# Optimization experiments

Measured on AMD Instinct MI355X. Metric: run time of the kernel, lower is better.

The kernel has to match this reference:

```python
import jax, jax.numpy as jnp
import numpy as np

HIDDEN = 1024
NHEAD = 16
HEAD_DIM = HIDDEN // NHEAD
B, S = 2, 2048


def setup_inputs() -> dict:
    key = jax.random.key(0)
    ks = jax.random.split(key, 10)
    scale = 1.0 / np.sqrt(HIDDEN)
    inp = {
        "x": jax.random.normal(ks[0], (B, S, HIDDEN), dtype=jnp.float32),
        "mask": jax.random.randint(ks[1], (B, S), 0, 2).astype(bool),
        "Wq": jax.random.normal(ks[2], (HIDDEN, HIDDEN), dtype=jnp.float32) * scale,
        "bq": jnp.zeros((HIDDEN,), dtype=jnp.float32),
        "Wk": jax.random.normal(ks[3], (HIDDEN, HIDDEN), dtype=jnp.float32) * scale,
        "bk": jnp.zeros((HIDDEN,), dtype=jnp.float32),
        "Wv": jax.random.normal(ks[4], (HIDDEN, HIDDEN), dtype=jnp.float32) * scale,
        "bv": jnp.zeros((HIDDEN,), dtype=jnp.float32),
        "Wo": jax.random.normal(ks[5], (HIDDEN, HIDDEN), dtype=jnp.float32) * scale,
        "bo": jnp.zeros((HIDDEN,), dtype=jnp.float32),
    }
    return inp


def reference(x, mask, Wq, bq, Wk, bk, Wv, bv, Wo, bo):
    B_, S_, H = x.shape
    # QKV projections (torch Linear: x @ W.T + b), split into heads -> [B, nhead, S, head_dim]
    def split_heads(t):
        return t.reshape(B_, S_, NHEAD, HEAD_DIM).transpose(0, 2, 1, 3)

    q = split_heads(x @ Wq.T + bq)
    k = split_heads(x @ Wk.T + bk)
    v = split_heads(x @ Wv.T + bv)

    # scaled dot-product scores: [B, nhead, S, S]
    energy = jnp.einsum("bhqd,bhkd->bhqk", q, k) / jnp.sqrt(jnp.float32(HEAD_DIM))

    # combined padding + diagonal-exclusion mask: mask keys where mask[b,k] is True,
    # but never mask the diagonal (self) position
    eye = jnp.eye(S_, dtype=bool)  # [S, S]
    attn_mask = mask[:, None, None, :] & ~eye[None, None, :, :]  # [B, 1, S, S] broadcast over heads
    energy = jnp.where(attn_mask, -jnp.inf, energy)

    attention = jax.nn.softmax(energy, axis=-1)
    out = jnp.einsum("bhqk,bhkd->bhqd", attention, v)  # [B, nhead, S, head_dim]
    out = out.transpose(0, 2, 1, 3).reshape(B_, S_, H)
    return out @ Wo.T + bo
```

## Files before the change

### kernel.cpp

```cpp
#include <hip/hip_runtime.h>

typedef __attribute__((ext_vector_type(8))) short short8;
typedef __attribute__((ext_vector_type(4))) float f32x4;
typedef __attribute__((ext_vector_type(16))) float f32x16;
typedef __attribute__((ext_vector_type(4))) unsigned short ushort4v;

#define HIDDEN 1024
#define NHEAD 16
#define HD 64
#define BATCH 2
#define SEQ 2048
#define MROWS (BATCH * SEQ)
#define QSCALE 0.18033688011112042f

__device__ __forceinline__ unsigned short f2b(float f) {
  union { float f; unsigned u; } v; v.f = f;
  unsigned r = v.u + 0x7fffu + ((v.u >> 16) & 1u);
  return (unsigned short)(r >> 16);
}

__device__ __forceinline__ unsigned cvt_pk_bf16(float lo, float hi) {
  unsigned r;
  asm("v_cvt_pk_bf16_f32 %0, %1, %2" : "=v"(r) : "v"(lo), "v"(hi));
  return r;
}

__device__ __forceinline__ float fexp2(float x) {
#if __has_builtin(__builtin_amdgcn_exp2f)
  return __builtin_amdgcn_exp2f(x);
#else
  return exp2f(x);
#endif
}

__device__ __forceinline__ void gll16(const void* g, void* l) {
  __builtin_amdgcn_global_load_lds(
      (__attribute__((address_space(1))) void*)g,
      (__attribute__((address_space(3))) void*)l, 16, 0, 0);
}

__global__ void prep_kernel(const float* __restrict__ x,
                            const float* __restrict__ Wq,
                            const float* __restrict__ Wk,
                            const float* __restrict__ Wv,
                            const float* __restrict__ Wo,
                            unsigned short* __restrict__ xb,
                            unsigned short* __restrict__ wqb,
                            unsigned short* __restrict__ wkb,
                            unsigned short* __restrict__ wvb,
                            unsigned short* __restrict__ wob) {
  int bid = blockIdx.x;
  const float* src;
  unsigned short* dst;
  int base;
  if (bid < 4096)      { src = x;  dst = xb;  base = bid; }
  else if (bid < 5120) { src = Wq; dst = wqb; base = bid - 4096; }
  else if (bid < 6144) { src = Wk; dst = wkb; base = bid - 5120; }
  else if (bid < 7168) { src = Wv; dst = wvb; base = bid - 6144; }
  else                 { src = Wo; dst = wob; base = bid - 7168; }
  int i = (base * 256 + threadIdx.x) * 4;
  float4 v = *reinterpret_cast<const float4*>(src + i);
  ushort4v o;
  o.x = f2b(v.x); o.y = f2b(v.y); o.z = f2b(v.z); o.w = f2b(v.w);
  *reinterpret_cast<ushort4v*>(dst + i) = o;
}

__global__ void amask_kernel(const int* __restrict__ m, float* __restrict__ am,
                             int n) {
  int i = blockIdx.x * blockDim.x + threadIdx.x;
  if (i < n) am[i] = m[i] ? -1e30f : 0.f;
}

template <int MODE>
__global__ __launch_bounds__(256) void gemm128_kernel(
    const unsigned short* __restrict__ A,
    const unsigned short* __restrict__ W0,
    const unsigned short* __restrict__ W1,
    const unsigned short* __restrict__ W2,
    const float* __restrict__ c0, const float* __restrict__ c1,
    const float* __restrict__ c2, void* __restrict__ o0,
    void* __restrict__ o1, void* __restrict__ o2) {
  __shared__ __align__(16) unsigned short Al[128 * 64];
  __shared__ __align__(16) unsigned short Bl[128 * 64];
  const int t = threadIdx.x;
  const int w = t >> 6, l = t & 63;
  const int hi = l >> 4, lo16 = l & 15;
  const int wr = w >> 1, wc = w & 1;
  const int m0 = blockIdx.x * 128;
  const int n0 = blockIdx.y * 128;
  const int K = HIDDEN;

  const unsigned short* Bsel;
  const float* bias;
  int region = 0, n_loc = n0;
  if (MODE == 0) {
    region = n0 >> 10;
    n_loc = n0 & 1023;
    Bsel = region == 0 ? W0 : (region == 1 ? W1 : W2);
    bias = region == 0 ? c0 : (region == 1 ? c1 : c2);
  } else {
    Bsel = W0;
    bias = c0;
  }

  const int srow = w * 32 + (l >> 3);
  const int schunk = (l & 7) ^ (l >> 3);
  const int rsw = (lo16 & 7);

  f32x4 acc[4][4];
#pragma unroll
  for (int mi = 0; mi < 4; ++mi)
#pragma unroll
    for (int f = 0; f < 4; ++f) acc[mi][f] = f32x4{0.f, 0.f, 0.f, 0.f};

  for (int kt = 0; kt < K; kt += 64) {
    __syncthreads();
#pragma unroll
    for (int i = 0; i < 4; ++i) {
      int r = srow + i * 8;
      gll16(A + (size_t)(m0 + r) * K + kt + schunk * 8,
            &Al[(w * 32 + i * 8) * 64]);
      gll16(Bsel + (size_t)(n_loc + r) * K + kt + schunk * 8,
            &Bl[(w * 32 + i * 8) * 64]);
    }
    __syncthreads();
#pragma unroll
    for (int kk = 0; kk < 2; ++kk) {
      short8 af[4], bf[4];
#pragma unroll
      for (int mi = 0; mi < 4; ++mi) {
        int row = wr * 64 + mi * 16 + lo16;
        af[mi] = *reinterpret_cast<const short8*>(
            &Al[row * 64 + (((kk * 4 + hi) ^ rsw) * 8)]);
      }
#pragma unroll
      for (int f = 0; f < 4; ++f) {
        int row = wc * 64 + f * 16 + lo16;
        bf[f] = *reinterpret_cast<const short8*>(
            &Bl[row * 64 + (((kk * 4 + hi) ^ rsw) * 8)]);
      }
#pragma unroll
      for (int mi = 0; mi < 4; ++mi)
#pragma unroll
        for (int f = 0; f < 4; ++f)
          acc[mi][f] =
              __builtin_amdgcn_mfma_f32_16x16x32_bf16(af[mi], bf[f], acc[mi][f], 0, 0, 0);
    }
  }

#pragma unroll
  for (int mi = 0; mi < 4; ++mi)
#pragma unroll
    for (int f = 0; f < 4; ++f) {
      int mbase = m0 + wr * 64 + mi * 16 + hi * 4;
      int n_rel = n_loc + wc * 64 + f * 16 + lo16;
      float bv_ = bias[n_rel];
#pragma unroll
      for (int j = 0; j < 4; ++j) {
        float v = acc[mi][f][j] + bv_;
        int mm = mbase + j;
        if (MODE == 0) {
          int b = mm >> 11, s = mm & 2047, h = n_rel >> 6, d = n_rel & 63;
          if (region == 0)
            ((unsigned short*)o0)[((size_t)(b * NHEAD + h) * SEQ + s) * HD + d] =
                f2b(v * QSCALE);
          else if (region == 1)
            ((unsigned short*)o1)[((size_t)(b * NHEAD + h) * SEQ + s) * HD + d] =
                f2b(v);
          else
            ((unsigned short*)o2)[((size_t)(b * NHEAD + h) * HD + d) * SEQ + s] =
                f2b(v);
        } else {
          ((float*)o0)[(size_t)mm * HIDDEN + n_rel] = v;
        }
      }
    }
}

__global__ __launch_bounds__(256) void attn_kernel(
    const unsigned short* __restrict__ Q, const unsigned short* __restrict__ Km,
    const unsigned short* __restrict__ Vt, const float* __restrict__ amf,
    unsigned short* __restrict__ O) {
  __shared__ __align__(16) unsigned short Kl[2][64 * 64];
  __shared__ __align__(16) unsigned short Vl[2][64 * 64];
  __shared__ __align__(16) float Am[SEQ];
  const int t = threadIdx.x;
  const int w = t >> 6, l = t & 63;
  const int q31 = l & 31, hi32 = l >> 5;
  const int bh = blockIdx.y;
  const int b = bh >> 4, h = bh & 15;
  const int q0w = blockIdx.x * 128 + w * 32;
  const int q = q0w + q31;
  const int dtile = q0w & ~63;

  const unsigned short* Qb = Q + (size_t)bh * SEQ * HD;
  const unsigned short* Kb = Km + (size_t)bh * SEQ * HD;
  const unsigned short* Vb = Vt + (size_t)bh * HD * SEQ;
  const float* mb = amf + b * SEQ;

  for (int i = t; i < SEQ / 4; i += 256)
    *reinterpret_cast<float4*>(&Am[i * 4]) =
        *reinterpret_cast<const float4*>(mb + i * 4);

  short8 qf[4];
#pragma unroll
  for (int dc = 0; dc < 4; ++dc)
    qf[dc] = *reinterpret_cast<const short8*>(
        Qb + (size_t)q * HD + dc * 16 + hi32 * 8);

  f32x16 o0, o1;
#pragma unroll
  for (int r = 0; r < 16; ++r) { o0[r] = 0.f; o1[r] = 0.f; }
  float srw = 0.f;

  const int srow = w * 16 + (l >> 3);
  const int sc0 = ((l & 7) ^ (l >> 3) ^ ((w * 2 + 0) & 3)) * 8;
  const int sc1 = ((l & 7) ^ (l >> 3) ^ ((w * 2 + 1) & 3)) * 8;
  const unsigned short* pK0 = Kb + (size_t)srow * HD + sc0;
  const unsigned short* pK1 = Kb + (size_t)(srow + 8) * HD + sc1;
  const unsigned short* pV0 = Vb + (size_t)srow * SEQ + sc0;
  const unsigned short* pV1 = Vb + (size_t)(srow + 8) * SEQ + sc1;

  gll16(pK0, &Kl[0][(w * 16 + 0) * 64]);
  gll16(pK1, &Kl[0][(w * 16 + 8) * 64]);
  gll16(pV0, &Vl[0][(w * 16 + 0) * 64]);
  gll16(pV1, &Vl[0][(w * 16 + 8) * 64]);
  pK0 += 64 * HD; pK1 += 64 * HD; pV0 += 64; pV1 += 64;
  __syncthreads();

  const int rk = (q31 & 7) ^ (q31 >> 3);

  auto step = [&](int k0, int BUF) __attribute__((always_inline)) {
    if (k0 + 64 < SEQ) {
      gll16(pK0, &Kl[BUF ^ 1][(w * 16 + 0) * 64]);
      gll16(pK1, &Kl[BUF ^ 1][(w * 16 + 8) * 64]);
      gll16(pV0, &Vl[BUF ^ 1][(w * 16 + 0) * 64]);
      gll16(pV1, &Vl[BUF ^ 1][(w * 16 + 8) * 64]);
      pK0 += 64 * HD; pK1 += 64 * HD; pV0 += 64; pV1 += 64;
    }

    f32x16 s0, s1;
    {
      float4 a0[4], a1[4];
#pragma unroll
      for (int g = 0; g < 4; ++g) {
        a0[g] = *reinterpret_cast<const float4*>(&Am[k0 + g * 8 + hi32 * 4]);
        a1[g] = *reinterpret_cast<const float4*>(&Am[k0 + 32 + g * 8 + hi32 * 4]);
      }
      if (k0 == dtile) {
        int kb = k0 + hi32 * 4;
#pragma unroll
        for (int g = 0; g < 4; ++g) {
          if (kb + g * 8 + 0 == q) a0[g].x = 0.f;
          if (kb + g * 8 + 1 == q) a0[g].y = 0.f;
          if (kb + g * 8 + 2 == q) a0[g].z = 0.f;
          if (kb + g * 8 + 3 == q) a0[g].w = 0.f;
          if (kb + g * 8 + 32 + 0 == q) a1[g].x = 0.f;
          if (kb + g * 8 + 32 + 1 == q) a1[g].y = 0.f;
          if (kb + g * 8 + 32 + 2 == q) a1[g].z = 0.f;
          if (kb + g * 8 + 32 + 3 == q) a1[g].w = 0.f;
        }
      }
#pragma unroll
      for (int g = 0; g < 4; ++g) {
        s0[4 * g + 0] = a0[g].x; s0[4 * g + 1] = a0[g].y;
        s0[4 * g + 2] = a0[g].z; s0[4 * g + 3] = a0[g].w;
        s1[4 * g + 0] = a1[g].x; s1[4 * g + 1] = a1[g].y;
        s1[4 * g + 2] = a1[g].z; s1[4 * g + 3] = a1[g].w;
      }
    }

    __builtin_amdgcn_s_setprio(1);
#pragma unroll
    for (int dc = 0; dc < 4; ++dc) {
      short8 k0f = *reinterpret_cast<const short8*>(
          &Kl[BUF][q31 * 64 + (((dc * 2 + hi32) ^ rk) * 8)]);
      short8 k1f = *reinterpret_cast<const short8*>(
          &Kl[BUF][(32 + q31) * 64 + (((dc * 2 + hi32) ^ rk) * 8)]);
      s0 = __builtin_amdgcn_mfma_f32_32x32x16_bf16(k0f, qf[dc], s0, 0, 0, 0);
      s1 = __builtin_amdgcn_mfma_f32_32x32x16_bf16(k1f, qf[dc], s1, 0, 0, 0);
    }
    __builtin_amdgcn_s_setprio(0);

    float sum = 0.f;
#pragma unroll
    for (int r = 0; r < 16; ++r) {
      float p0 = fexp2(s0[r]);
      float p1 = fexp2(s1[r]);
      s0[r] = p0; s1[r] = p1;
      sum += p0 + p1;
    }
    {
      unsigned a = __float_as_uint(sum), bsw = a;
      auto rr = __builtin_amdgcn_permlane32_swap(a, bsw, false, false);
      sum = __uint_as_float(rr[0]) + __uint_as_float(rr[1]);
    }
    srw += sum;

    unsigned c0[8], c1[8];
#pragma unroll
    for (int R = 0; R < 4; ++R) {
      c0[R * 2 + 0] = cvt_pk_bf16(s0[4 * R + 0], s0[4 * R + 1]);
      c0[R * 2 + 1] = cvt_pk_bf16(s0[4 * R + 2], s0[4 * R + 3]);
      c1[R * 2 + 0] = cvt_pk_bf16(s1[4 * R + 0], s1[4 * R + 1]);
      c1[R * 2 + 1] = cvt_pk_bf16(s1[4 * R + 2], s1[4 * R + 3]);
    }

    short8 pb[4];
#pragma unroll
    for (int s = 0; s < 4; ++s) {
      const unsigned* cc = (s < 2) ? c0 : c1;
      const int R0 = (s & 1) * 2;
      auto r0 = __builtin_amdgcn_permlane32_swap(cc[R0 * 2 + 0],
                                                 cc[(R0 + 1) * 2 + 0], false, false);
      auto r1 = __builtin_amdgcn_permlane32_swap(cc[R0 * 2 + 1],
                                                 cc[(R0 + 1) * 2 + 1], false, false);
      union { unsigned u[4]; short8 s8; } pu;
      pu.u[0] = r0[0]; pu.u[1] = r1[0]; pu.u[2] = r0[1]; pu.u[3] = r1[1];
      pb[s] = pu.s8;
    }

    __builtin_amdgcn_s_setprio(1);
#pragma unroll
    for (int s = 0; s < 4; ++s) {
      short8 vf = *reinterpret_cast<const short8*>(
          &Vl[BUF][q31 * 64 + (((s * 2 + hi32) ^ rk) * 8)]);
      o0 = __builtin_amdgcn_mfma_f32_32x32x16_bf16(vf, pb[s], o0, 0, 0, 0);
    }
#pragma unroll
    for (int s = 0; s < 4; ++s) {
      short8 vf = *reinterpret_cast<const short8*>(
          &Vl[BUF][(32 + q31) * 64 + (((s * 2 + hi32) ^ rk) * 8)]);
      o1 = __builtin_amdgcn_mfma_f32_32x32x16_bf16(vf, pb[s], o1, 0, 0, 0);
    }
    __builtin_amdgcn_s_setprio(0);

    __syncthreads();
  };

  for (int k0 = 0; k0 < SEQ; k0 += 128) {
    step(k0, 0);
    step(k0 + 64, 1);
  }

  float rinv = 1.f / srw;
  unsigned short* Ob = O + (size_t)(b * SEQ + q) * HIDDEN + h * HD;
#pragma unroll
  for (int g = 0; g < 4; ++g) {
    uint2 w0, w1;
    w0.x = cvt_pk_bf16(o0[4 * g + 0] * rinv, o0[4 * g + 1] * rinv);
    w0.y = cvt_pk_bf16(o0[4 * g + 2] * rinv, o0[4 * g + 3] * rinv);
    w1.x = cvt_pk_bf16(o1[4 * g + 0] * rinv, o1[4 * g + 1] * rinv);
    w1.y = cvt_pk_bf16(o1[4 * g + 2] * rinv, o1[4 * g + 3] * rinv);
    *reinterpret_cast<uint2*>(Ob + 8 * g + 4 * hi32) = w0;
    *reinterpret_cast<uint2*>(Ob + 32 + 8 * g + 4 * hi32) = w1;
  }
}

extern "C" void kernel_launch(void* const* d_in, const int* in_sizes, int n_in,
                              void* d_out, int out_size, void* d_ws,
                              size_t ws_size, hipStream_t stream) {
  const float* x = (const float*)d_in[0];
  const int* mask = (const int*)d_in[1];
  const float* Wq = (const float*)d_in[2];
  const float* bq = (const float*)d_in[3];
  const float* Wk = (const float*)d_in[4];
  const float* bk = (const float*)d_in[5];
  const float* Wv = (const float*)d_in[6];
  const float* bv = (const float*)d_in[7];
  const float* Wo = (const float*)d_in[8];
  const float* bo = (const float*)d_in[9];

  char* ws = (char*)d_ws;
  unsigned short* xb  = (unsigned short*)(ws + ((size_t)0 << 20));
  unsigned short* wqb = (unsigned short*)(ws + ((size_t)8 << 20));
  unsigned short* wkb = (unsigned short*)(ws + ((size_t)10 << 20));
  unsigned short* wvb = (unsigned short*)(ws + ((size_t)12 << 20));
  unsigned short* wob = (unsigned short*)(ws + ((size_t)14 << 20));
  unsigned short* qw  = (unsigned short*)(ws + ((size_t)16 << 20));
  unsigned short* kw  = (unsigned short*)(ws + ((size_t)24 << 20));
  unsigned short* vtw = (unsigned short*)(ws + ((size_t)32 << 20));
  unsigned short* ow  = (unsigned short*)(ws + ((size_t)40 << 20));
  float* amf = (float*)(ws + ((size_t)0 << 20));

  prep_kernel<<<8192, 256, 0, stream>>>(x, Wq, Wk, Wv, Wo, xb, wqb, wkb, wvb,
                                        wob);

  gemm128_kernel<0><<<dim3(MROWS / 128, 3 * HIDDEN / 128), 256, 0, stream>>>(
      xb, wqb, wkb, wvb, bq, bk, bv, qw, kw, vtw);

  amask_kernel<<<MROWS / 256, 256, 0, stream>>>(mask, amf, MROWS);

  attn_kernel<<<dim3(SEQ / 128, BATCH * NHEAD), 256, 0, stream>>>(qw, kw, vtw,
                                                                  amf, ow);

  gemm128_kernel<1><<<dim3(MROWS / 128, HIDDEN / 128), 256, 0, stream>>>(
      ow, wob, nullptr, nullptr, bo, nullptr, nullptr, d_out, nullptr, nullptr);
}
```

Measured before the change: 136.5 us.

## Double-buffer GEMM tiles and shrink attention blocks to two waves

The projection GEMM now double-buffers its A/B shared-memory tiles, issuing the next K-slice's global-to-LDS loads before computing on the current one, with one barrier per step instead of two. The attention kernel moves from 4 waves/128 queries to 2 waves/64 queries per block, so each wave loads more of the K/V tile and the grid doubles. It also reads the additive mask straight from global memory instead of staging it in LDS. The GEMM doubles its LDS footprint, which may reduce occupancy, and smaller attention blocks reread K/V more often in total.

```diff
diff --git a/kernel.cpp b/kernel.cpp
--- a/kernel.cpp
+++ b/kernel.cpp
@@ -80,8 +80,8 @@
     const float* __restrict__ c0, const float* __restrict__ c1,
     const float* __restrict__ c2, void* __restrict__ o0,
     void* __restrict__ o1, void* __restrict__ o2) {
-  __shared__ __align__(16) unsigned short Al[128 * 64];
-  __shared__ __align__(16) unsigned short Bl[128 * 64];
+  __shared__ __align__(16) unsigned short Al[2][128 * 64];
+  __shared__ __align__(16) unsigned short Bl[2][128 * 64];
   const int t = threadIdx.x;
   const int w = t >> 6, l = t & 63;
   const int hi = l >> 4, lo16 = l & 15;
@@ -107,23 +107,37 @@
   const int schunk = (l & 7) ^ (l >> 3);
   const int rsw = (lo16 & 7);
 
+  const unsigned short* pA[4];
+  const unsigned short* pB[4];
+#pragma unroll
+  for (int i = 0; i < 4; ++i) {
+    pA[i] = A + (size_t)(m0 + srow + i * 8) * K + schunk * 8;
+    pB[i] = Bsel + (size_t)(n_loc + srow + i * 8) * K + schunk * 8;
+  }
+
   f32x4 acc[4][4];
 #pragma unroll
   for (int mi = 0; mi < 4; ++mi)
 #pragma unroll
     for (int f = 0; f < 4; ++f) acc[mi][f] = f32x4{0.f, 0.f, 0.f, 0.f};
 
-  for (int kt = 0; kt < K; kt += 64) {
-    __syncthreads();
-#pragma unroll
-    for (int i = 0; i < 4; ++i) {
-      int r = srow + i * 8;
-      gll16(A + (size_t)(m0 + r) * K + kt + schunk * 8,
-            &Al[(w * 32 + i * 8) * 64]);
-      gll16(Bsel + (size_t)(n_loc + r) * K + kt + schunk * 8,
-            &Bl[(w * 32 + i * 8) * 64]);
-    }
-    __syncthreads();
+#pragma unroll
+  for (int i = 0; i < 4; ++i) {
+    gll16(pA[i], &Al[0][(w * 32 + i * 8) * 64]);
+    gll16(pB[i], &Bl[0][(w * 32 + i * 8) * 64]);
+    pA[i] += 64; pB[i] += 64;
+  }
+  __syncthreads();
+
+  auto step = [&](int knext, int BUF) __attribute__((always_inline)) {
+    if (knext < K) {
+#pragma unroll
+      for (int i = 0; i < 4; ++i) {
+        gll16(pA[i], &Al[BUF ^ 1][(w * 32 + i * 8) * 64]);
+        gll16(pB[i], &Bl[BUF ^ 1][(w * 32 + i * 8) * 64]);
+        pA[i] += 64; pB[i] += 64;
+      }
+    }
 #pragma unroll
     for (int kk = 0; kk < 2; ++kk) {
       short8 af[4], bf[4];
@@ -131,13 +145,13 @@
       for (int mi = 0; mi < 4; ++mi) {
         int row = wr * 64 + mi * 16 + lo16;
         af[mi] = *reinterpret_cast<const short8*>(
-            &Al[row * 64 + (((kk * 4 + hi) ^ rsw) * 8)]);
+            &Al[BUF][row * 64 + (((kk * 4 + hi) ^ rsw) * 8)]);
       }
 #pragma unroll
       for (int f = 0; f < 4; ++f) {
         int row = wc * 64 + f * 16 + lo16;
         bf[f] = *reinterpret_cast<const short8*>(
-            &Bl[row * 64 + (((kk * 4 + hi) ^ rsw) * 8)]);
+            &Bl[BUF][row * 64 + (((kk * 4 + hi) ^ rsw) * 8)]);
       }
 #pragma unroll
       for (int mi = 0; mi < 4; ++mi)
@@ -146,6 +160,12 @@
           acc[mi][f] =
               __builtin_amdgcn_mfma_f32_16x16x32_bf16(af[mi], bf[f], acc[mi][f], 0, 0, 0);
     }
+    __syncthreads();
+  };
+
+  for (int kt = 0; kt < K; kt += 128) {
+    step(kt + 64, 0);
+    step(kt + 128, 1);
   }
 
 #pragma unroll
@@ -177,31 +197,26 @@
     }
 }
 
-__global__ __launch_bounds__(256) void attn_kernel(
+__global__ __launch_bounds__(128) void attn_kernel(
     const unsigned short* __restrict__ Q, const unsigned short* __restrict__ Km,
     const unsigned short* __restrict__ Vt, const float* __restrict__ amf,
     unsigned short* __restrict__ O) {
   __shared__ __align__(16) unsigned short Kl[2][64 * 64];
   __shared__ __align__(16) unsigned short Vl[2][64 * 64];
-  __shared__ __align__(16) float Am[SEQ];
   const int t = threadIdx.x;
   const int w = t >> 6, l = t & 63;
   const int q31 = l & 31, hi32 = l >> 5;
   const int bh = blockIdx.y;
   const int b = bh >> 4, h = bh & 15;
-  const int q0w = blockIdx.x * 128 + w * 32;
+  const int q0w = blockIdx.x * 64 + w * 32;
   const int q = q0w + q31;
-  const int dtile = q0w & ~63;
+  const int dtile = blockIdx.x * 64;
 
   const unsigned short* Qb = Q + (size_t)bh * SEQ * HD;
   const unsigned short* Kb = Km + (size_t)bh * SEQ * HD;
   const unsigned short* Vb = Vt + (size_t)bh * HD * SEQ;
   const float* mb = amf + b * SEQ;
 
-  for (int i = t; i < SEQ / 4; i += 256)
-    *reinterpret_cast<float4*>(&Am[i * 4]) =
-        *reinterpret_cast<const float4*>(mb + i * 4);
-
   short8 qf[4];
 #pragma unroll
   for (int dc = 0; dc < 4; ++dc)
@@ -213,61 +228,64 @@
   for (int r = 0; r < 16; ++r) { o0[r] = 0.f; o1[r] = 0.f; }
   float srw = 0.f;
 
-  const int srow = w * 16 + (l >> 3);
-  const int sc0 = ((l & 7) ^ (l >> 3) ^ ((w * 2 + 0) & 3)) * 8;
-  const int sc1 = ((l & 7) ^ (l >> 3) ^ ((w * 2 + 1) & 3)) * 8;
-  const unsigned short* pK0 = Kb + (size_t)srow * HD + sc0;
-  const unsigned short* pK1 = Kb + (size_t)(srow + 8) * HD + sc1;
-  const unsigned short* pV0 = Vb + (size_t)srow * SEQ + sc0;
-  const unsigned short* pV1 = Vb + (size_t)(srow + 8) * SEQ + sc1;
-
-  gll16(pK0, &Kl[0][(w * 16 + 0) * 64]);
-  gll16(pK1, &Kl[0][(w * 16 + 8) * 64]);
-  gll16(pV0, &Vl[0][(w * 16 + 0) * 64]);
-  gll16(pV1, &Vl[0][(w * 16 + 8) * 64]);
-  pK0 += 64 * HD; pK1 += 64 * HD; pV0 += 64; pV1 += 64;
+  const unsigned short* pK[4];
+  const unsigned short* pV[4];
+#pragma unroll
+  for (int i = 0; i < 4; ++i) {
+    int row = w * 32 + i * 8 + (l >> 3);
+    int sc_ = ((l & 7) ^ (l >> 3) ^ i) * 8;
+    pK[i] = Kb + (size_t)row * HD + sc_;
+    pV[i] = Vb + (size_t)row * SEQ + sc_;
+  }
+
+#pragma unroll
+  for (int i = 0; i < 4; ++i) {
+    gll16(pK[i], &Kl[0][(w * 32 + i * 8) * 64]);
+    gll16(pV[i], &Vl[0][(w * 32 + i * 8) * 64]);
+    pK[i] += 64 * HD; pV[i] += 64;
+  }
   __syncthreads();
 
   const int rk = (q31 & 7) ^ (q31 >> 3);
 
   auto step = [&](int k0, int BUF) __attribute__((always_inline)) {
+    float4 a0[4], a1[4];
+#pragma unroll
+    for (int g = 0; g < 4; ++g) {
+      a0[g] = *reinterpret_cast<const float4*>(mb + k0 + g * 8 + hi32 * 4);
+      a1[g] = *reinterpret_cast<const float4*>(mb + k0 + 32 + g * 8 + hi32 * 4);
+    }
+
     if (k0 + 64 < SEQ) {
-      gll16(pK0, &Kl[BUF ^ 1][(w * 16 + 0) * 64]);
-      gll16(pK1, &Kl[BUF ^ 1][(w * 16 + 8) * 64]);
-      gll16(pV0, &Vl[BUF ^ 1][(w * 16 + 0) * 64]);
-      gll16(pV1, &Vl[BUF ^ 1][(w * 16 + 8) * 64]);
-      pK0 += 64 * HD; pK1 += 64 * HD; pV0 += 64; pV1 += 64;
+#pragma unroll
+      for (int i = 0; i < 4; ++i) {
+        gll16(pK[i], &Kl[BUF ^ 1][(w * 32 + i * 8) * 64]);
+        gll16(pV[i], &Vl[BUF ^ 1][(w * 32 + i * 8) * 64]);
+        pK[i] += 64 * HD; pV[i] += 64;
+      }
     }
 
     f32x16 s0, s1;
-    {
-      float4 a0[4], a1[4];
+    if (k0 == dtile) {
+      int kb = k0 + hi32 * 4;
 #pragma unroll
       for (int g = 0; g < 4; ++g) {
-        a0[g] = *reinterpret_cast<const float4*>(&Am[k0 + g * 8 + hi32 * 4]);
-        a1[g] = *reinterpret_cast<const float4*>(&Am[k0 + 32 + g * 8 + hi32 * 4]);
-      }
-      if (k0 == dtile) {
-        int kb = k0 + hi32 * 4;
-#pragma unroll
-        for (int g = 0; g < 4; ++g) {
-          if (kb + g * 8 + 0 == q) a0[g].x = 0.f;
-          if (kb + g * 8 + 1 == q) a0[g].y = 0.f;
-          if (kb + g * 8 + 2 == q) a0[g].z = 0.f;
-          if (kb + g * 8 + 3 == q) a0[g].w = 0.f;
-          if (kb + g * 8 + 32 + 0 == q) a1[g].x = 0.f;
-          if (kb + g * 8 + 32 + 1 == q) a1[g].y = 0.f;
-          if (kb + g * 8 + 32 + 2 == q) a1[g].z = 0.f;
-          if (kb + g * 8 + 32 + 3 == q) a1[g].w = 0.f;
-        }
-      }
-#pragma unroll
-      for (int g = 0; g < 4; ++g) {
-        s0[4 * g + 0] = a0[g].x; s0[4 * g + 1] = a0[g].y;
-        s0[4 * g + 2] = a0[g].z; s0[4 * g + 3] = a0[g].w;
-        s1[4 * g + 0] = a1[g].x; s1[4 * g + 1] = a1[g].y;
-        s1[4 * g + 2] = a1[g].z; s1[4 * g + 3] = a1[g].w;
-      }
+        if (kb + g * 8 + 0 == q) a0[g].x = 0.f;
+        if (kb + g * 8 + 1 == q) a0[g].y = 0.f;
+        if (kb + g * 8 + 2 == q) a0[g].z = 0.f;
+        if (kb + g * 8 + 3 == q) a0[g].w = 0.f;
+        if (kb + g * 8 + 32 + 0 == q) a1[g].x = 0.f;
+        if (kb + g * 8 + 32 + 1 == q) a1[g].y = 0.f;
+        if (kb + g * 8 + 32 + 2 == q) a1[g].z = 0.f;
+        if (kb + g * 8 + 32 + 3 == q) a1[g].w = 0.f;
+      }
+    }
+#pragma unroll
+    for (int g = 0; g < 4; ++g) {
+      s0[4 * g + 0] = a0[g].x; s0[4 * g + 1] = a0[g].y;
+      s0[4 * g + 2] = a0[g].z; s0[4 * g + 3] = a0[g].w;
+      s1[4 * g + 0] = a1[g].x; s1[4 * g + 1] = a1[g].y;
+      s1[4 * g + 2] = a1[g].z; s1[4 * g + 3] = a1[g].w;
     }
 
     __builtin_amdgcn_s_setprio(1);
@@ -391,8 +409,8 @@
 
   amask_kernel<<<MROWS / 256, 256, 0, stream>>>(mask, amf, MROWS);
 
-  attn_kernel<<<dim3(SEQ / 128, BATCH * NHEAD), 256, 0, stream>>>(qw, kw, vtw,
-                                                                  amf, ow);
+  attn_kernel<<<dim3(SEQ / 64, BATCH * NHEAD), 128, 0, stream>>>(qw, kw, vtw,
+                                                                 amf, ow);
 
   gemm128_kernel<1><<<dim3(MROWS / 128, HIDDEN / 128), 256, 0, stream>>>(
       ow, wob, nullptr, nullptr, bo, nullptr, nullptr, d_out, nullptr, nullptr);
```

New measurement: 145.7 us. +6.8%, slower.
